# Optimization experiments

Hardware: AMD Instinct MI355X
Metric: run time of the kernel (lower is better)

## Reference

```python
import jax, jax.numpy as jnp
import numpy as np

N_NODES = 50000
N_EDGES = 800000
D = 128
BN_EPS = 1e-5


def setup_inputs() -> dict:
    key = jax.random.key(0)
    k1, k2, k3, k4 = jax.random.split(key, 4)
    feature = jax.random.normal(k1, (N_NODES, D), dtype=jnp.float32)
    W = jax.random.normal(k2, (D, D), dtype=jnp.float32) * (1.0 / np.sqrt(D))
    b = jnp.zeros((D,), dtype=jnp.float32)
    gamma = jnp.ones((D,), dtype=jnp.float32)
    beta = jnp.zeros((D,), dtype=jnp.float32)
    src = jax.random.randint(k3, (N_EDGES,), 0, N_NODES, dtype=jnp.int64)
    dst = jax.random.randint(k4, (N_EDGES,), 0, N_NODES, dtype=jnp.int64)
    return {"feature": feature, "W": W, "b": b, "gamma": gamma, "beta": beta,
            "src": src, "dst": dst}


def reference(feature, W, b, gamma, beta, src, dst):
    # --- message passing: copy_u + mean over in-neighbors ---
    n = feature.shape[0]
    msgs = feature[src]  # [E, D] gather of source node features
    agg = jax.ops.segment_sum(msgs, dst, num_segments=n)  # [N, D]
    deg = jax.ops.segment_sum(jnp.ones((src.shape[0],), feature.dtype), dst,
                              num_segments=n)  # [N]
    h = jnp.where(deg[:, None] > 0, agg / jnp.maximum(deg, 1.0)[:, None], 0.0)
    # --- node apply: linear ---
    h = h @ W.T + b
    # --- BatchNorm1d (training mode: biased batch stats over node dim) ---
    mu = jnp.mean(h, axis=0)
    var = jnp.mean(jnp.square(h - mu), axis=0)
    h = (h - mu) / jnp.sqrt(var + BN_EPS) * gamma + beta
    # --- activation + residual (dropout p=0 is identity) ---
    h = jax.nn.relu(h)
    h = feature + h
    return h
```

## Files before the change

### kernel.cpp

```cpp
#include <hip/hip_runtime.h>
#include <cstddef>
#include <cstdint>

#define N_NODES 50000
#define N_EDGES 800000
#define D 128
#define BN_EPS 1e-5f

#define NBUCKET 782
#define BCAP 1536
#define PART_BLOCKS 128
#define PART_CHUNK 6250
#define SLOTS 48
#define SLOTS_P 50
#define GEMM_CHUNKS 1563
#define GEMM_GRID   512
#define FEAT_V8     (N_NODES * D / 8)
#define SLICE_V8    (N_NODES * 4)
#define W_V8        (D * D / 8)
#define CAST_BLOCKS ((FEAT_V8 + W_V8 + 255) / 256)
#define ZERO_V4     3192

typedef __attribute__((ext_vector_type(8))) short short8_t;
typedef __attribute__((ext_vector_type(8))) unsigned short u16x8;
typedef __attribute__((ext_vector_type(4))) float f32x4;
typedef __attribute__((ext_vector_type(4))) int i32x4;

#define WS_STAT_OFF    0
#define WS_GCUR_OFF    1024
#define WS_WB_OFF      51072
#define WS_CLAIM_OFF   83840
#define WS_HB_OFF      4888448
#define WS_FB_OFF      17688448

static __device__ __forceinline__ unsigned short f2bf(float x) {
    unsigned u = __float_as_uint(x);
    unsigned r = (u + 0x7fffu + ((u >> 16) & 1u)) >> 16;
    return (unsigned short)r;
}
static __device__ __forceinline__ float bf2f(unsigned short v) {
    return __uint_as_float(((unsigned)v) << 16);
}

__global__ __launch_bounds__(256) void prezero_k(i32x4* __restrict__ zws) {
    int i = blockIdx.x * 256 + threadIdx.x;
    if (i < ZERO_V4) zws[i] = (i32x4){0, 0, 0, 0};
}

__global__ __launch_bounds__(256) void castpart_k(const float* __restrict__ feat,
                                                  const float* __restrict__ W,
                                                  u16x8* __restrict__ fb,
                                                  u16x8* __restrict__ wb,
                                                  const int* __restrict__ src,
                                                  const int* __restrict__ dst,
                                                  int* __restrict__ gcur,
                                                  unsigned* __restrict__ claims) {
    __shared__ unsigned pk[PART_CHUNK];
    __shared__ int hist[NBUCKET];
    __shared__ int base_l[NBUCKET];
    const int t = threadIdx.x;

    if (blockIdx.x < PART_BLOCKS) {
        const int base = blockIdx.x * PART_CHUNK;

        for (int b = t; b < NBUCKET; b += 256) hist[b] = 0;
        __syncthreads();

        for (int i = t; i < PART_CHUNK; i += 256) {
            int s = src[base + i];
            int d = dst[base + i];
            pk[i] = ((unsigned)s << 16) | (unsigned)d;
            atomicAdd(&hist[d >> 6], 1);
        }
        __syncthreads();

        for (int b = t; b < NBUCKET; b += 256) {
            int h = hist[b];
            base_l[b] = h ? atomicAdd(gcur + b * 16, h) : 0;
            hist[b] = 0;
        }
        __syncthreads();

        for (int i = t; i < PART_CHUNK; i += 256) {
            unsigned u = pk[i];
            int bkt = (int)(u & 0xffffu) >> 6;
            int k = atomicAdd(&hist[bkt], 1);
            int pos = base_l[bkt] + k;
            if (pos < BCAP) claims[bkt * BCAP + pos] = u;
        }
    } else {
        int i = (blockIdx.x - PART_BLOCKS) * 256 + t;
        if (i < FEAT_V8) {
            int q  = i / SLICE_V8;
            int r  = i - q * SLICE_V8;
            int n  = r >> 2, oc = r & 3;
            const f32x4* fp = reinterpret_cast<const f32x4*>(feat + n * D + q * 32 + oc * 8);
            f32x4 x0 = __builtin_nontemporal_load(fp);
            f32x4 x1 = __builtin_nontemporal_load(fp + 1);
            u16x8 o;
            o[0] = f2bf(x0.x); o[1] = f2bf(x0.y); o[2] = f2bf(x0.z); o[3] = f2bf(x0.w);
            o[4] = f2bf(x1.x); o[5] = f2bf(x1.y); o[6] = f2bf(x1.z); o[7] = f2bf(x1.w);
            __builtin_nontemporal_store(o, fb + i);
        } else if (i < FEAT_V8 + W_V8) {
            int j = i - FEAT_V8;
            const f32x4* fp = reinterpret_cast<const f32x4*>(W) + j * 2;
            f32x4 x0 = __builtin_nontemporal_load(fp);
            f32x4 x1 = __builtin_nontemporal_load(fp + 1);
            u16x8 o;
            o[0] = f2bf(x0.x); o[1] = f2bf(x0.y); o[2] = f2bf(x0.z); o[3] = f2bf(x0.w);
            o[4] = f2bf(x1.x); o[5] = f2bf(x1.y); o[6] = f2bf(x1.z); o[7] = f2bf(x1.w);
            __builtin_nontemporal_store(o, wb + j);
        }
    }
}

__global__ __launch_bounds__(256) void bingather_k(const int* __restrict__ gcur,
                                                   const unsigned* __restrict__ claims,
                                                   const u16x8* __restrict__ fb,
                                                   u16x8* __restrict__ hb) {
    __shared__ unsigned short ebl[64 * SLOTS_P];
    __shared__ int lcnt[64];
    const int t = threadIdx.x;
    const int b = blockIdx.x >> 2;
    const int q = blockIdx.x & 3;
    const u16x8* fbq = fb + (size_t)q * SLICE_V8;

    if (t < 64) lcnt[t] = 0;
    __syncthreads();

    const int n = min(gcur[b * 16], BCAP);
    const unsigned* cp = claims + b * BCAP;
    for (int i = t; i < n; i += 256) {
        unsigned u = cp[i];
        int dl = (int)(u & 63u);
        int k = atomicAdd(&lcnt[dl], 1);
        if (k < SLOTS) ebl[dl * SLOTS_P + k] = (unsigned short)(u >> 16);
    }
    __syncthreads();

    const int nl = t >> 2;
    const int oc = t & 3;
    const int node = (b << 6) + nl;
    const int deg = lcnt[nl];
    const int nd  = min(deg, SLOTS);
    const unsigned short* slots = ebl + nl * SLOTS_P;

    float a[8];
#pragma unroll
    for (int i = 0; i < 8; ++i) a[i] = 0.f;

    int e = 0;
    for (; e + 2 <= nd; e += 2) {
        int s0 = slots[e], s1 = slots[e + 1];
        u16x8 v0 = fbq[s0 * 4 + oc];
        u16x8 v1 = fbq[s1 * 4 + oc];
#pragma unroll
        for (int i = 0; i < 8; ++i) a[i] += bf2f(v0[i]) + bf2f(v1[i]);
    }
    if (e < nd) {
        u16x8 v0 = fbq[(int)slots[e] * 4 + oc];
#pragma unroll
        for (int i = 0; i < 8; ++i) a[i] += bf2f(v0[i]);
    }

    if (node < N_NODES) {
        float inv = (deg > 0) ? 1.f / (float)deg : 0.f;
        u16x8 o;
#pragma unroll
        for (int i = 0; i < 8; ++i) o[i] = f2bf(a[i] * inv);
        hb[node * 16 + q * 4 + oc] = o;
    }
}

__global__ __launch_bounds__(256) void gemm_mfma_k(const u16x8* __restrict__ hb,
                                                   const u16x8* __restrict__ wb,
                                                   const float* __restrict__ bias,
                                                   float* __restrict__ h,
                                                   float* __restrict__ colsum,
                                                   float* __restrict__ colsumsq) {
    const int wave = threadIdx.x >> 6;
    const int lane = threadIdx.x & 63;
    const int wm = wave >> 1, wn = wave & 1;
    const int l15 = lane & 15, l4 = lane >> 4;

    short8_t bf[4][4];
#pragma unroll
    for (int t = 0; t < 4; ++t) {
        const int col = wn * 64 + t * 16 + l15;
#pragma unroll
        for (int s = 0; s < 4; ++s) {
            u16x8 w = wb[col * 16 + s * 4 + l4];
            short8_t b8;
#pragma unroll
            for (int i = 0; i < 8; ++i) b8[i] = (short)w[i];
            bf[t][s] = b8;
        }
    }
    float bc[4];
#pragma unroll
    for (int t = 0; t < 4; ++t) bc[t] = bias[wn * 64 + t * 16 + l15];

    float s1[4] = {0.f, 0.f, 0.f, 0.f};
    float s2[4] = {0.f, 0.f, 0.f, 0.f};

    for (int chunk = blockIdx.x; chunk < GEMM_CHUNKS; chunk += gridDim.x) {
        const int rbase = chunk * 32 + wm * 16;
        const int arow = min(rbase + l15, N_NODES - 1);
        const u16x8* ap = hb + arow * 16;
        short8_t af[4];
#pragma unroll
        for (int s = 0; s < 4; ++s) {
            u16x8 hv8 = ap[s * 4 + l4];
            short8_t t8;
#pragma unroll
            for (int i = 0; i < 8; ++i) t8[i] = (short)hv8[i];
            af[s] = t8;
        }

        f32x4 acc[4];
#pragma unroll
        for (int t = 0; t < 4; ++t) acc[t] = (f32x4){0.f, 0.f, 0.f, 0.f};

#pragma unroll
        for (int s = 0; s < 4; ++s)
#pragma unroll
            for (int t = 0; t < 4; ++t)
                acc[t] = __builtin_amdgcn_mfma_f32_16x16x32_bf16(af[s], bf[t][s],
                                                                 acc[t], 0, 0, 0);

        const int orow0 = rbase + l4 * 4;
#pragma unroll
        for (int t = 0; t < 4; ++t) {
            const int col = wn * 64 + t * 16 + l15;
#pragma unroll
            for (int r = 0; r < 4; ++r) {
                const int row = orow0 + r;
                if (row < N_NODES) {
                    float hv = acc[t][r] + bc[t];
                    h[(size_t)row * D + col] = hv;
                    s1[t] += hv;
                    s2[t] += hv * hv;
                }
            }
        }
    }

#pragma unroll
    for (int t = 0; t < 4; ++t) {
        s1[t] += __shfl_xor(s1[t], 16); s1[t] += __shfl_xor(s1[t], 32);
        s2[t] += __shfl_xor(s2[t], 16); s2[t] += __shfl_xor(s2[t], 32);
    }
    if (lane < 16) {
#pragma unroll
        for (int t = 0; t < 4; ++t) {
            int col = wn * 64 + t * 16 + lane;
            atomicAdd(colsum + col, s1[t]);
            atomicAdd(colsumsq + col, s2[t]);
        }
    }
}

__global__ __launch_bounds__(256) void epilogue_k(float* __restrict__ h,
                                                  const float* __restrict__ feat,
                                                  const float* __restrict__ colsum,
                                                  const float* __restrict__ colsumsq,
                                                  const float* __restrict__ gamma,
                                                  const float* __restrict__ beta) {
    int idx = blockIdx.x * blockDim.x + threadIdx.x;
    const int total = N_NODES * D / 4;
    if (idx >= total) return;
    int colb = (idx * 4) & 127;
    const float4 s1 = *reinterpret_cast<const float4*>(colsum + colb);
    const float4 s2 = *reinterpret_cast<const float4*>(colsumsq + colb);
    const float4 g  = *reinterpret_cast<const float4*>(gamma + colb);
    const float4 bt = *reinterpret_cast<const float4*>(beta + colb);
    const float inv_n = 1.0f / N_NODES;

    float4 a, bb;
    {
        float mu = s1.x * inv_n, var = s2.x * inv_n - mu * mu;
        float r = g.x * rsqrtf(var + BN_EPS); a.x = r; bb.x = bt.x - mu * r;
        mu = s1.y * inv_n; var = s2.y * inv_n - mu * mu;
        r = g.y * rsqrtf(var + BN_EPS); a.y = r; bb.y = bt.y - mu * r;
        mu = s1.z * inv_n; var = s2.z * inv_n - mu * mu;
        r = g.z * rsqrtf(var + BN_EPS); a.z = r; bb.z = bt.z - mu * r;
        mu = s1.w * inv_n; var = s2.w * inv_n - mu * mu;
        r = g.w * rsqrtf(var + BN_EPS); a.w = r; bb.w = bt.w - mu * r;
    }

    float4 hv = reinterpret_cast<float4*>(h)[idx];
    float4 fv = reinterpret_cast<const float4*>(feat)[idx];
    float4 o;
    o.x = fv.x + fmaxf(hv.x * a.x + bb.x, 0.f);
    o.y = fv.y + fmaxf(hv.y * a.y + bb.y, 0.f);
    o.z = fv.z + fmaxf(hv.z * a.z + bb.z, 0.f);
    o.w = fv.w + fmaxf(hv.w * a.w + bb.w, 0.f);
    reinterpret_cast<float4*>(h)[idx] = o;
}

extern "C" void kernel_launch(void* const* d_in, const int* in_sizes, int n_in,
                              void* d_out, int out_size, void* d_ws, size_t ws_size,
                              hipStream_t stream) {
    const float* feature = (const float*)d_in[0];
    const float* W       = (const float*)d_in[1];
    const float* b       = (const float*)d_in[2];
    const float* gamma   = (const float*)d_in[3];
    const float* beta    = (const float*)d_in[4];
    const int*   src     = (const int*)d_in[5];
    const int*   dst     = (const int*)d_in[6];
    float* out = (float*)d_out;

    char* ws = (char*)d_ws;
    float*    colsum   = (float*)(ws + WS_STAT_OFF);
    float*    colsumsq = colsum + 128;
    int*      gcur     = (int*)(ws + WS_GCUR_OFF);
    u16x8*    wb       = (u16x8*)(ws + WS_WB_OFF);
    unsigned* claims   = (unsigned*)(ws + WS_CLAIM_OFF);
    u16x8*    hb       = (u16x8*)(ws + WS_HB_OFF);
    u16x8*    fb       = (u16x8*)(ws + WS_FB_OFF);

    prezero_k<<<13, 256, 0, stream>>>((i32x4*)ws);
    castpart_k<<<PART_BLOCKS + CAST_BLOCKS, 256, 0, stream>>>(
        feature, W, fb, wb, src, dst, gcur, claims);
    bingather_k<<<NBUCKET * 4, 256, 0, stream>>>(gcur, claims, fb, hb);
    gemm_mfma_k<<<GEMM_GRID, 256, 0, stream>>>(hb, wb, b, out, colsum, colsumsq);
    epilogue_k<<<(N_NODES * D / 4 + 255) / 256, 256, 0, stream>>>(
        out, feature, colsum, colsumsq, gamma, beta);
}
```

Before: 108.2 us.

## Store GEMM output as bf16, slice-major hb layout, wider gather unroll, more partition blocks

```diff
diff --git a/kernel.cpp b/kernel.cpp
--- a/kernel.cpp
+++ b/kernel.cpp
@@ -9,8 +9,8 @@
 
 #define NBUCKET 782
 #define BCAP 1536
-#define PART_BLOCKS 128
-#define PART_CHUNK 6250
+#define PART_BLOCKS 256
+#define PART_CHUNK 3125
 #define SLOTS 48
 #define SLOTS_P 50
 #define GEMM_CHUNKS 1563
@@ -31,7 +31,8 @@
 #define WS_WB_OFF      51072
 #define WS_CLAIM_OFF   83840
 #define WS_HB_OFF      4888448
-#define WS_FB_OFF      17688448
+#define WS_H2_OFF      17688448
+#define WS_FB_OFF      30488448
 
 static __device__ __forceinline__ unsigned short f2bf(float x) {
     unsigned u = __float_as_uint(x);
@@ -150,14 +151,18 @@
     for (int i = 0; i < 8; ++i) a[i] = 0.f;
 
     int e = 0;
-    for (; e + 2 <= nd; e += 2) {
-        int s0 = slots[e], s1 = slots[e + 1];
+    for (; e + 4 <= nd; e += 4) {
+        int s0 = slots[e],     s1 = slots[e + 1];
+        int s2 = slots[e + 2], s3 = slots[e + 3];
         u16x8 v0 = fbq[s0 * 4 + oc];
         u16x8 v1 = fbq[s1 * 4 + oc];
-#pragma unroll
-        for (int i = 0; i < 8; ++i) a[i] += bf2f(v0[i]) + bf2f(v1[i]);
-    }
-    if (e < nd) {
+        u16x8 v2 = fbq[s2 * 4 + oc];
+        u16x8 v3 = fbq[s3 * 4 + oc];
+#pragma unroll
+        for (int i = 0; i < 8; ++i) a[i] += (bf2f(v0[i]) + bf2f(v1[i])) +
+                                            (bf2f(v2[i]) + bf2f(v3[i]));
+    }
+    for (; e < nd; ++e) {
         u16x8 v0 = fbq[(int)slots[e] * 4 + oc];
 #pragma unroll
         for (int i = 0; i < 8; ++i) a[i] += bf2f(v0[i]);
@@ -168,14 +173,14 @@
         u16x8 o;
 #pragma unroll
         for (int i = 0; i < 8; ++i) o[i] = f2bf(a[i] * inv);
-        hb[node * 16 + q * 4 + oc] = o;
+        hb[(size_t)q * SLICE_V8 + node * 4 + oc] = o;
     }
 }
 
 __global__ __launch_bounds__(256) void gemm_mfma_k(const u16x8* __restrict__ hb,
                                                    const u16x8* __restrict__ wb,
                                                    const float* __restrict__ bias,
-                                                   float* __restrict__ h,
+                                                   unsigned short* __restrict__ h2,
                                                    float* __restrict__ colsum,
                                                    float* __restrict__ colsumsq) {
     const int wave = threadIdx.x >> 6;
@@ -206,11 +211,10 @@
     for (int chunk = blockIdx.x; chunk < GEMM_CHUNKS; chunk += gridDim.x) {
         const int rbase = chunk * 32 + wm * 16;
         const int arow = min(rbase + l15, N_NODES - 1);
-        const u16x8* ap = hb + arow * 16;
         short8_t af[4];
 #pragma unroll
         for (int s = 0; s < 4; ++s) {
-            u16x8 hv8 = ap[s * 4 + l4];
+            u16x8 hv8 = hb[(size_t)s * SLICE_V8 + arow * 4 + l4];
             short8_t t8;
 #pragma unroll
             for (int i = 0; i < 8; ++i) t8[i] = (short)hv8[i];
@@ -237,7 +241,7 @@
                 const int row = orow0 + r;
                 if (row < N_NODES) {
                     float hv = acc[t][r] + bc[t];
-                    h[(size_t)row * D + col] = hv;
+                    h2[(size_t)row * D + col] = f2bf(hv);
                     s1[t] += hv;
                     s2[t] += hv * hv;
                 }
@@ -260,42 +264,37 @@
     }
 }
 
-__global__ __launch_bounds__(256) void epilogue_k(float* __restrict__ h,
+__global__ __launch_bounds__(256) void epilogue_k(const u16x8* __restrict__ h2v,
                                                   const float* __restrict__ feat,
                                                   const float* __restrict__ colsum,
                                                   const float* __restrict__ colsumsq,
                                                   const float* __restrict__ gamma,
-                                                  const float* __restrict__ beta) {
-    int idx = blockIdx.x * blockDim.x + threadIdx.x;
-    const int total = N_NODES * D / 4;
-    if (idx >= total) return;
-    int colb = (idx * 4) & 127;
-    const float4 s1 = *reinterpret_cast<const float4*>(colsum + colb);
-    const float4 s2 = *reinterpret_cast<const float4*>(colsumsq + colb);
-    const float4 g  = *reinterpret_cast<const float4*>(gamma + colb);
-    const float4 bt = *reinterpret_cast<const float4*>(beta + colb);
+                                                  const float* __restrict__ beta,
+                                                  float* __restrict__ out) {
+    int idx = blockIdx.x * 256 + threadIdx.x;
+    if (idx >= FEAT_V8) return;
+    const int colb = (idx * 8) & 127;
     const float inv_n = 1.0f / N_NODES;
 
-    float4 a, bb;
-    {
-        float mu = s1.x * inv_n, var = s2.x * inv_n - mu * mu;
-        float r = g.x * rsqrtf(var + BN_EPS); a.x = r; bb.x = bt.x - mu * r;
-        mu = s1.y * inv_n; var = s2.y * inv_n - mu * mu;
-        r = g.y * rsqrtf(var + BN_EPS); a.y = r; bb.y = bt.y - mu * r;
-        mu = s1.z * inv_n; var = s2.z * inv_n - mu * mu;
-        r = g.z * rsqrtf(var + BN_EPS); a.z = r; bb.z = bt.z - mu * r;
-        mu = s1.w * inv_n; var = s2.w * inv_n - mu * mu;
-        r = g.w * rsqrtf(var + BN_EPS); a.w = r; bb.w = bt.w - mu * r;
-    }
-
-    float4 hv = reinterpret_cast<float4*>(h)[idx];
-    float4 fv = reinterpret_cast<const float4*>(feat)[idx];
-    float4 o;
-    o.x = fv.x + fmaxf(hv.x * a.x + bb.x, 0.f);
-    o.y = fv.y + fmaxf(hv.y * a.y + bb.y, 0.f);
-    o.z = fv.z + fmaxf(hv.z * a.z + bb.z, 0.f);
-    o.w = fv.w + fmaxf(hv.w * a.w + bb.w, 0.f);
-    reinterpret_cast<float4*>(h)[idx] = o;
+    u16x8 hv8 = h2v[idx];
+    const float4* fp = reinterpret_cast<const float4*>(feat) + idx * 2;
+    float4 fv0 = fp[0], fv1 = fp[1];
+    float4 o0, o1;
+#pragma unroll
+    for (int i = 0; i < 8; ++i) {
+        int c = colb + i;
+        float mu  = colsum[c] * inv_n;
+        float var = colsumsq[c] * inv_n - mu * mu;
+        float a   = gamma[c] * rsqrtf(var + BN_EPS);
+        float bb  = beta[c] - mu * a;
+        float hv  = bf2f(hv8[i]);
+        float fv  = (i < 4) ? (&fv0.x)[i] : (&fv1.x)[i - 4];
+        float ov  = fv + fmaxf(hv * a + bb, 0.f);
+        if (i < 4) (&o0.x)[i] = ov; else (&o1.x)[i - 4] = ov;
+    }
+    float4* op = reinterpret_cast<float4*>(out) + idx * 2;
+    op[0] = o0;
+    op[1] = o1;
 }
 
 extern "C" void kernel_launch(void* const* d_in, const int* in_sizes, int n_in,
@@ -311,19 +310,20 @@
     float* out = (float*)d_out;
 
     char* ws = (char*)d_ws;
-    float*    colsum   = (float*)(ws + WS_STAT_OFF);
-    float*    colsumsq = colsum + 128;
-    int*      gcur     = (int*)(ws + WS_GCUR_OFF);
-    u16x8*    wb       = (u16x8*)(ws + WS_WB_OFF);
-    unsigned* claims   = (unsigned*)(ws + WS_CLAIM_OFF);
-    u16x8*    hb       = (u16x8*)(ws + WS_HB_OFF);
-    u16x8*    fb       = (u16x8*)(ws + WS_FB_OFF);
+    float*          colsum   = (float*)(ws + WS_STAT_OFF);
+    float*          colsumsq = colsum + 128;
+    int*            gcur     = (int*)(ws + WS_GCUR_OFF);
+    u16x8*          wb       = (u16x8*)(ws + WS_WB_OFF);
+    unsigned*       claims   = (unsigned*)(ws + WS_CLAIM_OFF);
+    u16x8*          hb       = (u16x8*)(ws + WS_HB_OFF);
+    unsigned short* h2       = (unsigned short*)(ws + WS_H2_OFF);
+    u16x8*          fb       = (u16x8*)(ws + WS_FB_OFF);
 
     prezero_k<<<13, 256, 0, stream>>>((i32x4*)ws);
     castpart_k<<<PART_BLOCKS + CAST_BLOCKS, 256, 0, stream>>>(
         feature, W, fb, wb, src, dst, gcur, claims);
     bingather_k<<<NBUCKET * 4, 256, 0, stream>>>(gcur, claims, fb, hb);
-    gemm_mfma_k<<<GEMM_GRID, 256, 0, stream>>>(hb, wb, b, out, colsum, colsumsq);
-    epilogue_k<<<(N_NODES * D / 4 + 255) / 256, 256, 0, stream>>>(
-        out, feature, colsum, colsumsq, gamma, beta);
-}
+    gemm_mfma_k<<<GEMM_GRID, 256, 0, stream>>>(hb, wb, b, h2, colsum, colsumsq);
+    epilogue_k<<<(FEAT_V8 + 255) / 256, 256, 0, stream>>>(
+        (u16x8*)h2, feature, colsum, colsumsq, gamma, beta, out);
+}
```

After: 105.3 us. -2.6%, faster.
